# Kernel optimization log

Measured on AMD Instinct MI355X. Metric: run time of the kernel, lower is better.

## Reference

```python
import jax, jax.numpy as jnp
import numpy as np

UNIT = 1024    # n_nodes == GRU hidden size (required: attention matmul needs fea == unit)
TSTEP = 128    # GRU input_size (time_step)
BATCH = 32
ALPHA = 0.2    # LeakyReLU negative slope


def setup_inputs() -> dict:
    key = jax.random.key(0)
    ks = jax.random.split(key, 7)
    s = 1.0 / np.sqrt(UNIT)  # torch GRU init scale
    return {
        "x": jax.random.normal(ks[0], (BATCH, TSTEP, UNIT), jnp.float32),
        "w_ih": jax.random.uniform(ks[1], (3 * UNIT, TSTEP), jnp.float32, -s, s),
        "w_hh": jax.random.uniform(ks[2], (3 * UNIT, UNIT), jnp.float32, -s, s),
        "b_ih": jax.random.uniform(ks[3], (3 * UNIT,), jnp.float32, -s, s),
        "b_hh": jax.random.uniform(ks[4], (3 * UNIT,), jnp.float32, -s, s),
        "weight_key": jax.random.normal(ks[5], (UNIT, 1), jnp.float32) * 0.05,
        "weight_query": jax.random.normal(ks[6], (UNIT, 1), jnp.float32) * 0.05,
    }


def _gru(xs, w_ih, w_hh, b_ih, b_hh):
    """torch-style GRU. xs: [S, B, I] -> outputs [S, B, H]. Gate order: r, z, n."""
    H = w_hh.shape[1]
    gi = jnp.einsum('sbi,gi->sbg', xs, w_ih) + b_ih  # precompute input gates [S,B,3H]

    def step(h, gi_t):
        gh = h @ w_hh.T + b_hh
        i_r, i_z, i_n = jnp.split(gi_t, 3, axis=-1)
        h_r, h_z, h_n = jnp.split(gh, 3, axis=-1)
        r = jax.nn.sigmoid(i_r + h_r)
        z = jax.nn.sigmoid(i_z + h_z)
        n = jnp.tanh(i_n + r * h_n)
        h_new = (1.0 - z) * n + z * h
        return h_new, h_new

    h0 = jnp.zeros((xs.shape[1], H), xs.dtype)
    _, out = jax.lax.scan(step, h0, gi)
    return out


def reference(x, w_ih, w_hh, b_ih, b_hh, weight_key, weight_query):
    # x: [B, T, N] -> GRU scans over the node axis with T features per node
    xs = jnp.transpose(x, (2, 0, 1))                 # [N, B, T]
    out = _gru(xs, w_ih, w_hh, b_ih, b_hh)           # [N, B, H]
    inp = jnp.transpose(out, (1, 0, 2))              # [B, N, H]

    # self_graph_attention (input.permute(0,2,1); H == N by construction)
    ip = jnp.transpose(inp, (0, 2, 1))               # [B, H, N]
    key_v = (ip @ weight_key)[..., 0]                # [B, N]
    qry_v = (ip @ weight_query)[..., 0]              # [B, N]
    # data[b,i,j] = key[b,i] + query[b,j]  (outer sum, same as repeat/view in torch)
    data = key_v[:, :, None] + qry_v[:, None, :]
    data = jnp.where(data > 0, data, ALPHA * data)   # LeakyReLU
    attention = jax.nn.softmax(data, axis=2)         # dropout == identity (eval)

    attention = jnp.mean(attention, axis=0)          # [N, N]
    degree = jnp.sum(attention, axis=1)
    attention = 0.5 * (attention + attention.T)
    d_inv = 1.0 / (jnp.sqrt(degree) + 1e-7)
    # diag(d_inv) @ (diag(degree) - A) @ diag(d_inv) as row/col scaling
    lap = d_inv[:, None] * (jnp.diag(degree) - attention) * d_inv[None, :]

    # Chebyshev polynomial chain, K = 4
    N = lap.shape[0]
    L0 = jnp.zeros((N, N), lap.dtype)
    L1 = lap
    L2 = 2.0 * (lap @ L1) - L0
    L3 = 2.0 * (lap @ L2) - L1
    mul_L = jnp.stack([L0, L1, L2, L3], axis=0)      # [4, N, N]
    return mul_L, attention
```

## Files before the change

kernel.cpp:

```cpp
#include <hip/hip_runtime.h>

#define H_    1024
#define T_    128
#define B_    32
#define S_    1024
#define NB_   64
#define JB_   16
#define KS_   36
#define NN_   (1024*1024)

typedef float f32x4 __attribute__((ext_vector_type(4)));
typedef __bf16 bf16x8 __attribute__((ext_vector_type(8)));

union FragU { uint4 q; bf16x8 v; unsigned short u[8]; };

static __device__ __forceinline__ unsigned short f2bf(float x) {
  unsigned u = __float_as_uint(x);
  u = (u + 0x7FFFu + ((u >> 16) & 1u)) >> 16;
  return (unsigned short)u;
}
static __device__ __forceinline__ float sigm(float x) { return 1.f / (1.f + __expf(-x)); }
static __device__ __forceinline__ float tanh_(float x) {
  float a = fabsf(x);
  float e = __expf(2.f * a);
  float t = 1.f - 2.f / (e + 1.f);
  return copysignf(t, x);
}
static __device__ __forceinline__ float lrelu(float x) { return x > 0.f ? x : 0.2f * x; }

static __device__ __forceinline__ void gld_lds16_c(const void* g, void* l) {
  __builtin_amdgcn_global_load_lds(
      (const __attribute__((address_space(1))) void*)g,
      (__attribute__((address_space(3))) void*)l, 16, 0, 0);
}
static __device__ __forceinline__ void gld_lds16_cc(const void* g, void* l) {
  __builtin_amdgcn_global_load_lds(
      (const __attribute__((address_space(1))) void*)g,
      (__attribute__((address_space(3))) void*)l, 16, 0, 17);
}

__global__ __launch_bounds__(256) void k_transpose(const float* __restrict__ x,
                                                   unsigned short* __restrict__ xT) {
  __shared__ float tile[128][65];
  int b  = blockIdx.x >> 4;
  int n0 = (blockIdx.x & 15) * 64;
  int tid = threadIdx.x;
  int sub = tid >> 6, nn = tid & 63;
  for (int it = 0; it < 32; ++it) {
    int t = it * 4 + sub;
    tile[t][nn] = x[(size_t)(b * 128 + t) * 1024 + n0 + nn];
  }
  __syncthreads();
  int nl = tid >> 7, tt = tid & 127;
  for (int it = 0; it < 32; ++it) {
    int n = it * 2 + nl;
    xT[(size_t)(n0 + n) * 4096 + (tt >> 4) * 512 + b * 16 + (tt & 15)] = f2bf(tile[tt][n]);
  }
}

__global__ __launch_bounds__(512) void k_gru(
    const float* __restrict__ w_ih, const float* __restrict__ w_hh,
    const float* __restrict__ b_ih, const float* __restrict__ b_hh,
    const float* __restrict__ wkey, const float* __restrict__ wqry,
    const unsigned short* __restrict__ xT,
    unsigned short* __restrict__ h_buf,
    int* __restrict__ done_blk,
    float* __restrict__ key_v, float* __restrict__ qry_v)
{
  __shared__ unsigned short h_sm[72][520];
  __shared__ float gh_lds[B_][65];
  __shared__ float wk_lds[S_], wq_lds[S_];

  const int tid  = threadIdx.x;
  const int bid  = blockIdx.x;
  const int lane = tid & 63;
  const int wave = tid >> 6;
  const int j0   = bid * JB_;

  for (int i = tid; i < S_; i += 512) { wk_lds[i] = wkey[i]; wq_lds[i] = wqry[i]; }

  const int mtile = wave & 1;
  const int ntile = wave >> 1;
  bf16x8 wfrag[KS_];
  if (wave < 6) {
    int col = lane & 15, kg = lane >> 4;
    int grow = ntile * H_ + j0 + col;
    for (int ks = 0; ks < KS_; ++ks) {
      int k = ks * 32 + kg * 8;
      const float* p = (k < H_) ? (w_hh + (size_t)grow * H_ + k)
                                : (w_ih + (size_t)grow * T_ + (k - H_));
      FragU cv;
      #pragma unroll
      for (int e = 0; e < 8; ++e) cv.u[e] = f2bf(p[e]);
      wfrag[ks] = cv.v;
    }
  }

  const int ejl = tid & 15;
  const int eb  = tid >> 4;
  const float bs_r = b_ih[j0 + ejl]          + b_hh[j0 + ejl];
  const float bs_z = b_ih[H_ + j0 + ejl]     + b_hh[H_ + j0 + ejl];
  const float bn_i = b_ih[2 * H_ + j0 + ejl];
  const float bn_h = b_hh[2 * H_ + j0 + ejl];

  float hreg = 0.f;
  float kacc = 0.f, qacc = 0.f;
  int spin_budget = 16000000;

  const int pbase = wave * 8;
  const int fl    = pbase + (lane & 7);

  for (int s = 0; s < S_; ++s) {
    const unsigned short* hprev = h_buf + ((s + 1) & 1) * (NB_ * 512);

    gld_lds16_c(xT + (size_t)s * 4096 + wave * 512 + lane * 8, &h_sm[64 + wave][0]);

    {
      unsigned pend = 0xFFu;
      while (pend) {
        int v = __hip_atomic_load(&done_blk[fl], __ATOMIC_RELAXED, __HIP_MEMORY_SCOPE_AGENT);
        unsigned r8 = (unsigned)__ballot(v >= s) & pend & 0xFFu;
        while (r8) {
          int i = __ffs(r8) - 1; r8 &= r8 - 1; pend &= ~(1u << i);
          int p = pbase + i;
          gld_lds16_cc(hprev + p * 512 + lane * 8, &h_sm[p][0]);
        }
        if (pend) {
          __builtin_amdgcn_s_sleep(1);
          if (--spin_budget < 0) pend = 0;
        }
      }
    }
    asm volatile("s_waitcnt vmcnt(0)" ::: "memory");
    __syncthreads();

    if (wave < 6) {
      const int abase = (mtile * 16 + (lane & 15)) * 16 + ((lane >> 4) & 1) * 8;
      const int ksl   = lane >> 5;
      if (ntile < 2) {
        f32x4 a0 = {0.f,0.f,0.f,0.f}, a1 = {0.f,0.f,0.f,0.f};
        #pragma unroll
        for (int ks = 0; ks < KS_; ks += 2) {
          FragU fa, fb;
          fa.q = *(const uint4*)&h_sm[2 * ks       + ksl][abase];
          fb.q = *(const uint4*)&h_sm[2 * (ks + 1) + ksl][abase];
          a0 = __builtin_amdgcn_mfma_f32_16x16x32_bf16(fa.v, wfrag[ks],     a0, 0, 0, 0);
          a1 = __builtin_amdgcn_mfma_f32_16x16x32_bf16(fb.v, wfrag[ks + 1], a1, 0, 0, 0);
        }
        f32x4 acc = a0 + a1;
        int dc = ntile * 16 + (lane & 15);
        int br = mtile * 16 + ((lane >> 4) << 2);
        #pragma unroll
        for (int r = 0; r < 4; ++r) gh_lds[br + r][dc] = acc[r];
      } else {
        f32x4 a0 = {0.f,0.f,0.f,0.f}, a1 = {0.f,0.f,0.f,0.f}, ax = {0.f,0.f,0.f,0.f};
        #pragma unroll
        for (int ks = 0; ks < 32; ks += 2) {
          FragU fa, fb;
          fa.q = *(const uint4*)&h_sm[2 * ks       + ksl][abase];
          fb.q = *(const uint4*)&h_sm[2 * (ks + 1) + ksl][abase];
          a0 = __builtin_amdgcn_mfma_f32_16x16x32_bf16(fa.v, wfrag[ks],     a0, 0, 0, 0);
          a1 = __builtin_amdgcn_mfma_f32_16x16x32_bf16(fb.v, wfrag[ks + 1], a1, 0, 0, 0);
        }
        #pragma unroll
        for (int ks = 32; ks < 36; ++ks) {
          FragU fa;
          fa.q = *(const uint4*)&h_sm[2 * ks + ksl][abase];
          ax = __builtin_amdgcn_mfma_f32_16x16x32_bf16(fa.v, wfrag[ks], ax, 0, 0, 0);
        }
        f32x4 acc = a0 + a1;
        int cc = lane & 15;
        int br = mtile * 16 + ((lane >> 4) << 2);
        #pragma unroll
        for (int r = 0; r < 4; ++r) {
          gh_lds[br + r][32 + cc] = acc[r];
          gh_lds[br + r][48 + cc] = ax[r];
        }
      }
    }
    __syncthreads();

    {
      float rs = gh_lds[eb][ejl]      + bs_r;
      float zs = gh_lds[eb][16 + ejl] + bs_z;
      float nh = gh_lds[eb][32 + ejl] + bn_h;
      float nx = gh_lds[eb][48 + ejl] + bn_i;
      float r  = sigm(rs);
      float z  = sigm(zs);
      float n  = tanh_(nx + r * nh);
      float hn = (1.f - z) * n + z * hreg;
      hreg = hn;
      kacc += wk_lds[s] * hn;
      qacc += wq_lds[s] * hn;
      unsigned int hb = (unsigned int)f2bf(hn);
      unsigned int ob = __shfl_xor(hb, 1);
      if ((tid & 1) == 0) {
        unsigned short* hcur = h_buf + (s & 1) * (NB_ * 512);
        unsigned int word = hb | (ob << 16);
        unsigned int* dst = (unsigned int*)(hcur + bid * 512 + tid);
        __hip_atomic_store(dst, word, __ATOMIC_RELAXED, __HIP_MEMORY_SCOPE_AGENT);
      }
    }
    asm volatile("s_waitcnt vmcnt(0)" ::: "memory");
    __syncthreads();

    if (tid == 0)
      __hip_atomic_store(&done_blk[bid], s + 1, __ATOMIC_RELAXED, __HIP_MEMORY_SCOPE_AGENT);
  }

  key_v[eb * H_ + j0 + ejl] = kacc;
  qry_v[eb * H_ + j0 + ejl] = qacc;
}

__global__ __launch_bounds__(256) void k_qmax(const float* __restrict__ qry_v,
                                              float* __restrict__ qmax) {
  int b = blockIdx.x, tid = threadIdx.x;
  float m = -1e30f;
  for (int i = tid; i < 1024; i += 256) m = fmaxf(m, qry_v[b * 1024 + i]);
  #pragma unroll
  for (int off = 32; off; off >>= 1) m = fmaxf(m, __shfl_xor(m, off));
  __shared__ float red[4];
  if ((tid & 63) == 0) red[tid >> 6] = m;
  __syncthreads();
  if (tid == 0) qmax[b] = fmaxf(fmaxf(red[0], red[1]), fmaxf(red[2], red[3]));
}

__global__ __launch_bounds__(256) void k_denom(const float* __restrict__ key_v,
                                               const float* __restrict__ qry_v,
                                               const float* __restrict__ qmax,
                                               float* __restrict__ mrow,
                                               float* __restrict__ rden) {
  int tid = threadIdx.x, lane = tid & 63;
  int row = blockIdx.x * 4 + (tid >> 6);
  int b = row >> 10;
  float k  = key_v[row];
  float mx = lrelu(k + qmax[b]);
  float sum = 0.f;
  for (int j = lane; j < 1024; j += 64)
    sum += __expf(lrelu(k + qry_v[b * 1024 + j]) - mx);
  #pragma unroll
  for (int off = 32; off; off >>= 1) sum += __shfl_xor(sum, off);
  if (lane == 0) { mrow[row] = mx; rden[row] = 1.f / sum; }
}

__global__ __launch_bounds__(256) void k_amean(const float* __restrict__ key_v,
                                               const float* __restrict__ qry_v,
                                               const float* __restrict__ mrow,
                                               const float* __restrict__ rden,
                                               float* __restrict__ A,
                                               float* __restrict__ degree) {
  __shared__ float qs[32][33];
  __shared__ float ks[32][9], ms[32][9], rs[32][9];
  int tid = threadIdx.x;
  int it = blockIdx.x >> 5, jt = blockIdx.x & 31;
  int i0 = it * 8, j0 = jt * 32;
  #pragma unroll
  for (int c = 0; c < 4; ++c) {
    int idx = tid + c * 256;
    int b = idx >> 5, j = idx & 31;
    qs[b][j] = qry_v[b * 1024 + j0 + j];
  }
  { int b = tid >> 3, ii = tid & 7;
    ks[b][ii] = key_v[b * 1024 + i0 + ii];
    ms[b][ii] = mrow[b * 1024 + i0 + ii];
    rs[b][ii] = rden[b * 1024 + i0 + ii]; }
  __syncthreads();
  int il = tid >> 5, jl = tid & 31;
  float acc = 0.f;
  #pragma unroll 4
  for (int b = 0; b < 32; ++b)
    acc += __expf(lrelu(ks[b][il] + qs[b][jl]) - ms[b][il]) * rs[b][il];
  acc *= (1.f / 32.f);
  A[(size_t)(i0 + il) * 1024 + j0 + jl] = acc;
  float v = acc;
  #pragma unroll
  for (int off = 16; off; off >>= 1) v += __shfl_xor(v, off);
  if (jl == 0) atomicAdd(&degree[i0 + il], v);
}

__global__ __launch_bounds__(256) void k_lap(const float* __restrict__ A,
                                             const float* __restrict__ degree,
                                             float* __restrict__ lap,
                                             float* __restrict__ att) {
  __shared__ float ta[32][33], tb[32][33];
  int it = blockIdx.x >> 5, jt = blockIdx.x & 31;
  int i0 = it * 32, j0 = jt * 32;
  int tid = threadIdx.x;
  int r = tid >> 5, c = tid & 31;
  for (int rr = r; rr < 32; rr += 8) {
    ta[rr][c] = A[(size_t)(i0 + rr) * 1024 + j0 + c];
    tb[rr][c] = A[(size_t)(j0 + rr) * 1024 + i0 + c];
  }
  __syncthreads();
  for (int rr = r; rr < 32; rr += 8) {
    int i = i0 + rr, j = j0 + c;
    float asym = 0.5f * (ta[rr][c] + tb[c][rr]);
    float di = 1.f / (sqrtf(degree[i]) + 1e-7f);
    float dj = 1.f / (sqrtf(degree[j]) + 1e-7f);
    float lv = di * dj * (((i == j) ? degree[i] : 0.f) - asym);
    att[(size_t)i * 1024 + j] = asym;
    lap[(size_t)i * 1024 + j] = lv;
  }
}

__global__ __launch_bounds__(256) void k_gemm(const float* __restrict__ A,
                                              const float* __restrict__ B,
                                              float* __restrict__ C, float alpha,
                                              const float* __restrict__ sub) {
  __shared__ float As[16][68], Bs[16][68];
  int it = blockIdx.x >> 4, jt = blockIdx.x & 15;
  int i0 = it * 64, j0 = jt * 64;
  int tid = threadIdx.x;
  float acc[4][4] = {};
  int rb = (tid >> 4) * 4, cb = (tid & 15) * 4;
  int arow = tid >> 2, akk = (tid & 3) * 4;
  int brow = tid >> 4, bjc = (tid & 15) * 4;
  for (int kt = 0; kt < 64; ++kt) {
    float4 av = *(const float4*)&A[(size_t)(i0 + arow) * 1024 + kt * 16 + akk];
    float4 bv = *(const float4*)&B[(size_t)(kt * 16 + brow) * 1024 + j0 + bjc];
    As[akk + 0][arow] = av.x; As[akk + 1][arow] = av.y;
    As[akk + 2][arow] = av.z; As[akk + 3][arow] = av.w;
    *(float4*)&Bs[brow][bjc] = bv;
    __syncthreads();
    #pragma unroll
    for (int k = 0; k < 16; ++k) {
      float4 a4 = *(const float4*)&As[k][rb];
      float4 b4 = *(const float4*)&Bs[k][cb];
      float aa[4] = {a4.x, a4.y, a4.z, a4.w};
      float bb[4] = {b4.x, b4.y, b4.z, b4.w};
      #pragma unroll
      for (int rr = 0; rr < 4; ++rr)
        #pragma unroll
        for (int cc = 0; cc < 4; ++cc) acc[rr][cc] += aa[rr] * bb[cc];
    }
    __syncthreads();
  }
  #pragma unroll
  for (int rr = 0; rr < 4; ++rr)
    #pragma unroll
    for (int cc = 0; cc < 4; ++cc) {
      size_t idx = (size_t)(i0 + rb + rr) * 1024 + j0 + cb + cc;
      float v = alpha * acc[rr][cc];
      if (sub) v -= sub[idx];
      C[idx] = v;
    }
}

extern "C" void kernel_launch(void* const* d_in, const int* in_sizes, int n_in,
                              void* d_out, int out_size, void* d_ws, size_t ws_size,
                              hipStream_t stream) {
  const float* x    = (const float*)d_in[0];
  const float* w_ih = (const float*)d_in[1];
  const float* w_hh = (const float*)d_in[2];
  const float* b_ih = (const float*)d_in[3];
  const float* b_hh = (const float*)d_in[4];
  const float* wkey = (const float*)d_in[5];
  const float* wqry = (const float*)d_in[6];
  float* out = (float*)d_out;

  char* ws = (char*)d_ws;
  unsigned short* xT   = (unsigned short*)(ws);
  unsigned short* hbuf = (unsigned short*)(ws + 8388608);
  int*   done          = (int*)          (ws + 8519680);
  float* key_v         = (float*)        (ws + 8523776);
  float* qry_v         = (float*)        (ws + 8654848);
  float* qmax          = (float*)        (ws + 8785920);
  float* mrow          = (float*)        (ws + 8790016);
  float* rden          = (float*)        (ws + 8921088);
  float* degree        = (float*)        (ws + 9052160);
  float* A             = (float*)        (ws + 9056256);

  (void)hipMemsetAsync(hbuf, 0, 131072 + 4096, stream);
  (void)hipMemsetAsync(degree, 0, 4096, stream);
  (void)hipMemsetAsync(out, 0, (size_t)NN_ * 4, stream);

  k_transpose<<<512, 256, 0, stream>>>(x, xT);
  k_gru<<<NB_, 512, 0, stream>>>(w_ih, w_hh, b_ih, b_hh, wkey, wqry, xT, hbuf, done, key_v, qry_v);
  k_qmax<<<32, 256, 0, stream>>>(qry_v, qmax);
  k_denom<<<8192, 256, 0, stream>>>(key_v, qry_v, qmax, mrow, rden);
  k_amean<<<4096, 256, 0, stream>>>(key_v, qry_v, mrow, rden, A, degree);
  k_lap<<<1024, 256, 0, stream>>>(A, degree, out + NN_, out + (size_t)4 * NN_);
  k_gemm<<<256, 256, 0, stream>>>(out + NN_, out + NN_, out + (size_t)2 * NN_, 2.f, nullptr);
  k_gemm<<<256, 256, 0, stream>>>(out + NN_, out + (size_t)2 * NN_, out + (size_t)3 * NN_, 2.f, out + NN_);
}
```

Before: 4.911 ms.

## Replace per-block done flags with tagged 64-bit hidden-state messages in GRU

```diff
diff --git a/kernel.cpp b/kernel.cpp
--- a/kernel.cpp
+++ b/kernel.cpp
@@ -32,11 +32,6 @@
   __builtin_amdgcn_global_load_lds(
       (const __attribute__((address_space(1))) void*)g,
       (__attribute__((address_space(3))) void*)l, 16, 0, 0);
-}
-static __device__ __forceinline__ void gld_lds16_cc(const void* g, void* l) {
-  __builtin_amdgcn_global_load_lds(
-      (const __attribute__((address_space(1))) void*)g,
-      (__attribute__((address_space(3))) void*)l, 16, 0, 17);
 }
 
 __global__ __launch_bounds__(256) void k_transpose(const float* __restrict__ x,
@@ -63,11 +58,10 @@
     const float* __restrict__ b_ih, const float* __restrict__ b_hh,
     const float* __restrict__ wkey, const float* __restrict__ wqry,
     const unsigned short* __restrict__ xT,
-    unsigned short* __restrict__ h_buf,
-    int* __restrict__ done_blk,
+    unsigned long long* __restrict__ h_msg,
     float* __restrict__ key_v, float* __restrict__ qry_v)
 {
-  __shared__ unsigned short h_sm[72][520];
+  __shared__ unsigned short h_sm[80][520];
   __shared__ float gh_lds[B_][65];
   __shared__ float wk_lds[S_], wq_lds[S_];
 
@@ -105,55 +99,65 @@
 
   float hreg = 0.f;
   float kacc = 0.f, qacc = 0.f;
-  int spin_budget = 16000000;
+  int spin_budget = 2000000;
 
   const int pbase = wave * 8;
-  const int fl    = pbase + (lane & 7);
+
+  gld_lds16_c(xT + wave * 512 + lane * 8, &h_sm[64 + wave][0]);
 
   for (int s = 0; s < S_; ++s) {
-    const unsigned short* hprev = h_buf + ((s + 1) & 1) * (NB_ * 512);
-
-    gld_lds16_c(xT + (size_t)s * 4096 + wave * 512 + lane * 8, &h_sm[64 + wave][0]);
-
     {
-      unsigned pend = 0xFFu;
-      while (pend) {
-        int v = __hip_atomic_load(&done_blk[fl], __ATOMIC_RELAXED, __HIP_MEMORY_SCOPE_AGENT);
-        unsigned r8 = (unsigned)__ballot(v >= s) & pend & 0xFFu;
-        while (r8) {
-          int i = __ffs(r8) - 1; r8 &= r8 - 1; pend &= ~(1u << i);
-          int p = pbase + i;
-          gld_lds16_cc(hprev + p * 512 + lane * 8, &h_sm[p][0]);
-        }
-        if (pend) {
-          __builtin_amdgcn_s_sleep(1);
-          if (--spin_budget < 0) pend = 0;
-        }
+      const unsigned tag = (unsigned)s;
+      const unsigned long long* src =
+          h_msg + (size_t)((s + 1) & 1) * (NB_ * 256) + (size_t)pbase * 256 + lane * 4;
+
+      unsigned long long v00, v01, v02, v03, v10, v11, v12, v13;
+      unsigned long long v20, v21, v22, v23, v30, v31, v32, v33;
+      unsigned long long v40, v41, v42, v43, v50, v51, v52, v53;
+      unsigned long long v60, v61, v62, v63, v70, v71, v72, v73;
+
+      #define LDV(p,q) v##p##q = __hip_atomic_load(src + (p)*256 + (q), __ATOMIC_RELAXED, __HIP_MEMORY_SCOPE_AGENT)
+      #define LD4(p) LDV(p,0); LDV(p,1); LDV(p,2); LDV(p,3)
+      LD4(0); LD4(1); LD4(2); LD4(3); LD4(4); LD4(5); LD4(6); LD4(7);
+
+      unsigned pend = 0xFFFFFFFFu;
+      #define CKV(p,q) if ((unsigned)(v##p##q >> 32) == tag) pend &= ~(1u << ((p)*4+(q)))
+      #define CK4(p) CKV(p,0); CKV(p,1); CKV(p,2); CKV(p,3)
+      CK4(0); CK4(1); CK4(2); CK4(3); CK4(4); CK4(5); CK4(6); CK4(7);
+
+      while (__any(pend)) {
+        if (--spin_budget < 0) break;
+        #define RLV(p,q) if (pend & (1u << ((p)*4+(q)))) { LDV(p,q); }
+        #define RL4(p) RLV(p,0); RLV(p,1); RLV(p,2); RLV(p,3)
+        RL4(0); RL4(1); RL4(2); RL4(3); RL4(4); RL4(5); RL4(6); RL4(7);
+        CK4(0); CK4(1); CK4(2); CK4(3); CK4(4); CK4(5); CK4(6); CK4(7);
       }
-    }
-    asm volatile("s_waitcnt vmcnt(0)" ::: "memory");
+
+      #define WRV(p) { uint4 w; w.x = (unsigned)v##p##0; w.y = (unsigned)v##p##1; \
+                       w.z = (unsigned)v##p##2; w.w = (unsigned)v##p##3; \
+                       *(uint4*)&h_sm[pbase + (p)][8 * lane] = w; }
+      WRV(0); WRV(1); WRV(2); WRV(3); WRV(4); WRV(5); WRV(6); WRV(7);
+      #undef LDV
+      #undef LD4
+      #undef CKV
+      #undef CK4
+      #undef RLV
+      #undef RL4
+      #undef WRV
+    }
+
+    if (s + 1 < S_)
+      gld_lds16_c(xT + (size_t)(s + 1) * 4096 + wave * 512 + lane * 8,
+                  &h_sm[64 + 8 * ((s + 1) & 1) + wave][0]);
+
     __syncthreads();
 
     if (wave < 6) {
       const int abase = (mtile * 16 + (lane & 15)) * 16 + ((lane >> 4) & 1) * 8;
       const int ksl   = lane >> 5;
+      const int xb    = 64 + 8 * (s & 1);
       if (ntile < 2) {
         f32x4 a0 = {0.f,0.f,0.f,0.f}, a1 = {0.f,0.f,0.f,0.f};
-        #pragma unroll
-        for (int ks = 0; ks < KS_; ks += 2) {
-          FragU fa, fb;
-          fa.q = *(const uint4*)&h_sm[2 * ks       + ksl][abase];
-          fb.q = *(const uint4*)&h_sm[2 * (ks + 1) + ksl][abase];
-          a0 = __builtin_amdgcn_mfma_f32_16x16x32_bf16(fa.v, wfrag[ks],     a0, 0, 0, 0);
-          a1 = __builtin_amdgcn_mfma_f32_16x16x32_bf16(fb.v, wfrag[ks + 1], a1, 0, 0, 0);
-        }
-        f32x4 acc = a0 + a1;
-        int dc = ntile * 16 + (lane & 15);
-        int br = mtile * 16 + ((lane >> 4) << 2);
-        #pragma unroll
-        for (int r = 0; r < 4; ++r) gh_lds[br + r][dc] = acc[r];
-      } else {
-        f32x4 a0 = {0.f,0.f,0.f,0.f}, a1 = {0.f,0.f,0.f,0.f}, ax = {0.f,0.f,0.f,0.f};
         #pragma unroll
         for (int ks = 0; ks < 32; ks += 2) {
           FragU fa, fb;
@@ -163,10 +167,31 @@
           a1 = __builtin_amdgcn_mfma_f32_16x16x32_bf16(fb.v, wfrag[ks + 1], a1, 0, 0, 0);
         }
         #pragma unroll
-        for (int ks = 32; ks < 36; ++ks) {
+        for (int kx = 0; kx < 4; ++kx) {
           FragU fa;
-          fa.q = *(const uint4*)&h_sm[2 * ks + ksl][abase];
-          ax = __builtin_amdgcn_mfma_f32_16x16x32_bf16(fa.v, wfrag[ks], ax, 0, 0, 0);
+          fa.q = *(const uint4*)&h_sm[xb + 2 * kx + ksl][abase];
+          a0 = __builtin_amdgcn_mfma_f32_16x16x32_bf16(fa.v, wfrag[32 + kx], a0, 0, 0, 0);
+        }
+        f32x4 acc = a0 + a1;
+        int dc = ntile * 16 + (lane & 15);
+        int br = mtile * 16 + ((lane >> 4) << 2);
+        #pragma unroll
+        for (int r = 0; r < 4; ++r) gh_lds[br + r][dc] = acc[r];
+      } else {
+        f32x4 a0 = {0.f,0.f,0.f,0.f}, a1 = {0.f,0.f,0.f,0.f}, ax = {0.f,0.f,0.f,0.f};
+        #pragma unroll
+        for (int ks = 0; ks < 32; ks += 2) {
+          FragU fa, fb;
+          fa.q = *(const uint4*)&h_sm[2 * ks       + ksl][abase];
+          fb.q = *(const uint4*)&h_sm[2 * (ks + 1) + ksl][abase];
+          a0 = __builtin_amdgcn_mfma_f32_16x16x32_bf16(fa.v, wfrag[ks],     a0, 0, 0, 0);
+          a1 = __builtin_amdgcn_mfma_f32_16x16x32_bf16(fb.v, wfrag[ks + 1], a1, 0, 0, 0);
+        }
+        #pragma unroll
+        for (int kx = 0; kx < 4; ++kx) {
+          FragU fa;
+          fa.q = *(const uint4*)&h_sm[xb + 2 * kx + ksl][abase];
+          ax = __builtin_amdgcn_mfma_f32_16x16x32_bf16(fa.v, wfrag[32 + kx], ax, 0, 0, 0);
         }
         f32x4 acc = a0 + a1;
         int cc = lane & 15;
@@ -192,20 +217,16 @@
       hreg = hn;
       kacc += wk_lds[s] * hn;
       qacc += wq_lds[s] * hn;
-      unsigned int hb = (unsigned int)f2bf(hn);
+      unsigned int hb = (unsigned)f2bf(hn);
       unsigned int ob = __shfl_xor(hb, 1);
       if ((tid & 1) == 0) {
-        unsigned short* hcur = h_buf + (s & 1) * (NB_ * 512);
-        unsigned int word = hb | (ob << 16);
-        unsigned int* dst = (unsigned int*)(hcur + bid * 512 + tid);
-        __hip_atomic_store(dst, word, __ATOMIC_RELAXED, __HIP_MEMORY_SCOPE_AGENT);
+        unsigned long long word =
+            ((unsigned long long)(unsigned)(s + 1) << 32) |
+            (unsigned long long)(hb | (ob << 16));
+        __hip_atomic_store(h_msg + (size_t)(s & 1) * (NB_ * 256) + (size_t)bid * 256 + (tid >> 1),
+                           word, __ATOMIC_RELAXED, __HIP_MEMORY_SCOPE_AGENT);
       }
     }
-    asm volatile("s_waitcnt vmcnt(0)" ::: "memory");
-    __syncthreads();
-
-    if (tid == 0)
-      __hip_atomic_store(&done_blk[bid], s + 1, __ATOMIC_RELAXED, __HIP_MEMORY_SCOPE_AGENT);
   }
 
   key_v[eb * H_ + j0 + ejl] = kacc;
@@ -359,23 +380,22 @@
   float* out = (float*)d_out;
 
   char* ws = (char*)d_ws;
-  unsigned short* xT   = (unsigned short*)(ws);
-  unsigned short* hbuf = (unsigned short*)(ws + 8388608);
-  int*   done          = (int*)          (ws + 8519680);
-  float* key_v         = (float*)        (ws + 8523776);
-  float* qry_v         = (float*)        (ws + 8654848);
-  float* qmax          = (float*)        (ws + 8785920);
-  float* mrow          = (float*)        (ws + 8790016);
-  float* rden          = (float*)        (ws + 8921088);
-  float* degree        = (float*)        (ws + 9052160);
-  float* A             = (float*)        (ws + 9056256);
-
-  (void)hipMemsetAsync(hbuf, 0, 131072 + 4096, stream);
+  unsigned short* xT        = (unsigned short*)(ws);
+  unsigned long long* h_msg = (unsigned long long*)(ws + 8388608);
+  float* key_v              = (float*)(ws + 8650752);
+  float* qry_v              = (float*)(ws + 8781824);
+  float* qmax               = (float*)(ws + 8912896);
+  float* mrow               = (float*)(ws + 8916992);
+  float* rden               = (float*)(ws + 9048064);
+  float* degree             = (float*)(ws + 9179136);
+  float* A                  = (float*)(ws + 9183232);
+
+  (void)hipMemsetAsync(h_msg, 0, 262144, stream);
   (void)hipMemsetAsync(degree, 0, 4096, stream);
   (void)hipMemsetAsync(out, 0, (size_t)NN_ * 4, stream);
 
   k_transpose<<<512, 256, 0, stream>>>(x, xT);
-  k_gru<<<NB_, 512, 0, stream>>>(w_ih, w_hh, b_ih, b_hh, wkey, wqry, xT, hbuf, done, key_v, qry_v);
+  k_gru<<<NB_, 512, 0, stream>>>(w_ih, w_hh, b_ih, b_hh, wkey, wqry, xT, h_msg, key_v, qry_v);
   k_qmax<<<32, 256, 0, stream>>>(qry_v, qmax);
   k_denom<<<8192, 256, 0, stream>>>(key_v, qry_v, qmax, mrow, rden);
   k_amean<<<4096, 256, 0, stream>>>(key_v, qry_v, mrow, rden, A, degree);
```

Result: slower. 10.91 ms (+122.2%).
